# Performance work log

Hardware: AMD Instinct MI355X
Metric: run time of the kernel (lower is better)

## Reference

```python
import jax, jax.numpy as jnp
import numpy as np

VOCAB, EMB, HID, LAYERS, SEQ, BATCH = 10000, 1024, 1024, 2, 64, 64


def setup_inputs() -> dict:
    key = jax.random.key(0)
    ks = jax.random.split(key, 12)
    b = 1.0 / np.sqrt(HID)
    u = lambda k, shape, bd: jax.random.uniform(k, shape, jnp.float32, -bd, bd)
    return {
        "inputs": jax.random.randint(ks[0], (SEQ, BATCH), 0, VOCAB),
        "hidden": jnp.zeros((LAYERS, BATCH, HID), jnp.float32),
        "emb": u(ks[1], (VOCAB, EMB), 0.1),
        "W0": u(ks[2], (EMB, 3 * HID), b),
        "U0": u(ks[3], (HID, 3 * HID), b),
        "bw0": u(ks[4], (3 * HID,), b),
        "bu0": u(ks[5], (3 * HID,), b),
        "W1": u(ks[6], (HID, 3 * HID), b),
        "U1": u(ks[7], (HID, 3 * HID), b),
        "bw1": u(ks[8], (3 * HID,), b),
        "bu1": u(ks[9], (3 * HID,), b),
        "fcW": u(ks[10], (VOCAB, HID), 0.1),
        "fcb": jnp.zeros((VOCAB,), jnp.float32),
    }


def gru_cell(x, h, W, U, bw, bu):
    gx = x @ W + bw            # [B, 3H]
    gh = h @ U + bu            # [B, 3H]
    i_r, i_z, i_n = jnp.split(gx, 3, axis=1)
    h_r, h_z, h_n = jnp.split(gh, 3, axis=1)
    r = jax.nn.sigmoid(i_r + h_r)
    z = jax.nn.sigmoid(i_z + h_z)
    h_tilde = jnp.tanh(i_n + r * h_n)
    return (1.0 - z) * h + z * h_tilde


def reference(inputs, hidden, emb, W0, U0, bw0, bu0, W1, U1, bw1, bu1, fcW, fcb):
    # dp_keep_prob = 1.0 -> dropout is identity (eval-mode reference)
    def step(hid, tok):
        x = emb[tok]                                   # [B, EMB]
        h0 = gru_cell(x, hid[0], W0, U0, bw0, bu0)     # [B, H]
        h1 = gru_cell(h0, hid[1], W1, U1, bw1, bu1)    # [B, H]
        y = h1 @ fcW.T + fcb                           # [B, V]
        return jnp.stack([h0, h1]), y

    hidden_f, logits = jax.lax.scan(step, hidden, inputs)
    return logits, hidden_f
```

## Files before the change

kernel.cpp:

```cpp
#include <hip/hip_runtime.h>
#include <math.h>

#define SEQL 64
#define BATCHN 64
#define HID 1024
#define EMBD 1024
#define VOCAB 10000
#define G3 3072
#define NPAD 10240
#define AROWS 4096
#define HSLOT 65536

typedef float f4v __attribute__((ext_vector_type(4)));
typedef unsigned short us4 __attribute__((ext_vector_type(4)));
typedef unsigned short us8 __attribute__((ext_vector_type(8)));
typedef __bf16 bf8v __attribute__((ext_vector_type(8)));

__device__ __forceinline__ unsigned short f2bf(float f) {
    unsigned u = __float_as_uint(f);
    u += 0x7fffu + ((u >> 16) & 1u);
    return (unsigned short)(u >> 16);
}
__device__ __forceinline__ float bf2f(unsigned short h) {
    return __uint_as_float(((unsigned)h) << 16);
}
__device__ __forceinline__ void split2(float f, unsigned short &hi, unsigned short &lo) {
    hi = f2bf(f);
    lo = f2bf(f - bf2f(hi));
}
__device__ __forceinline__ f4v mfma16(us8 a, us8 b, f4v c) {
    return __builtin_amdgcn_mfma_f32_16x16x32_bf16(
        __builtin_bit_cast(bf8v, a), __builtin_bit_cast(bf8v, b), c, 0, 0, 0);
}
__device__ __forceinline__ float sigmoidf_(float x) { return 1.f / (1.f + expf(-x)); }

__device__ __forceinline__ size_t htile_off(int b, int j) {
    return ((size_t)((((b >> 4) * 32 + (j >> 5)) * 64) + ((j >> 3) & 3) * 16 + (b & 15))) * 8 + (j & 7);
}

__global__ __launch_bounds__(256)
void tile_weights_kernel(const float* __restrict__ U0, const float* __restrict__ W1,
                         const float* __restrict__ U1, const float* __restrict__ W0,
                         unsigned short* __restrict__ hi, unsigned short* __restrict__ lo)
{
    __shared__ float tile[32][65];
    const int mat = blockIdx.z;
    const float* src = (mat == 0) ? U0 : (mat == 1) ? W1 : (mat == 2) ? U1 : W0;
    const int n0 = blockIdx.x * 64, k0 = blockIdx.y * 32;
    const int t = threadIdx.x, tx = t & 63, ty = t >> 6;
#pragma unroll
    for (int s = 0; s < 8; s++)
        tile[ty * 8 + s][tx] = src[(size_t)(k0 + ty * 8 + s) * G3 + n0 + tx];
    __syncthreads();
    const int c = t >> 6, lane = t & 63, fr = lane & 15, kg = lane >> 4;
    const int cc = (n0 >> 4) + c;
    const size_t off = (((size_t)(mat * 192 + cc) * 32 + (k0 >> 5)) * 64 + lane) * 8;
    us8 h8, l8;
#pragma unroll
    for (int e = 0; e < 8; e++) {
        unsigned short a, b;
        split2(tile[kg * 8 + e][c * 16 + fr], a, b);
        h8[e] = a; l8[e] = b;
    }
    *(us8*)(hi + off) = h8;
    *(us8*)(lo + off) = l8;
}

__global__ void fc_pad_split_kernel(const float* __restrict__ fcW,
                                    unsigned short* __restrict__ hi, unsigned short* __restrict__ lo,
                                    const float* __restrict__ fcb, float* __restrict__ fcb_pad)
{
    size_t g = (size_t)blockIdx.x * 256 + threadIdx.x;
    if (g < NPAD) fcb_pad[g] = (g < VOCAB) ? fcb[g] : 0.f;
    size_t i = g * 4;
    size_t row = i >> 10;
    f4v v = {0.f, 0.f, 0.f, 0.f};
    if (row < VOCAB) v = *(const f4v*)(fcW + i);
    us4 h, l;
#pragma unroll
    for (int j = 0; j < 4; j++) { unsigned short a, b; split2(v[j], a, b); h[j] = a; l[j] = b; }
    *(us4*)(hi + i) = h;
    *(us4*)(lo + i) = l;
}

__global__ void small_prep_kernel(const float* __restrict__ hidden,
                                  unsigned short* __restrict__ h0th, unsigned short* __restrict__ h0tl,
                                  unsigned short* __restrict__ h1th, unsigned short* __restrict__ h1tl)
{
    int idx = blockIdx.x * 256 + threadIdx.x;
    if (idx < BATCHN * HID) {
        int b = idx >> 10, j = idx & 1023;
        size_t o = htile_off(b, j);
        unsigned short a1, b1;
        split2(hidden[idx], a1, b1);                 h0th[o] = a1; h0tl[o] = b1;
        split2(hidden[BATCHN * HID + idx], a1, b1);  h1th[o] = a1; h1tl[o] = b1;
    }
}

__global__ __launch_bounds__(256)
void gx0_gemm_kernel(const int* __restrict__ tok, const float* __restrict__ emb,
                     const unsigned short* __restrict__ Wthi, const unsigned short* __restrict__ Wtlo,
                     float* __restrict__ C)
{
    __shared__ unsigned short Ah[128][40], Al[128][40];
    const int bswz = blockIdx.x;
    const int xcd = bswz & 7, s = bswz >> 3;
    const int col0 = (xcd + 8 * (s >> 5)) * 128;
    const int row0 = (s & 31) * 128;
    const int tid = threadIdx.x;
    const int lane = tid & 63, wave = tid >> 6;
    const int wm = wave >> 1, wn = wave & 1;
    const int srow = tid >> 1;
    const int shalf = (tid & 1) * 16;

    const float* asrc = emb + (size_t)tok[row0 + srow] * EMBD + shalf;
    const int fr = lane & 15, fk = (lane >> 4) * 8;
    const int cc0 = (col0 >> 4) + wn * 4;

    f4v a[4];
#pragma unroll
    for (int q = 0; q < 4; q++) a[q] = *(const f4v*)(asrc + q * 4);

    f4v acc[4][4] = {};
    for (int k0 = 0; k0 < EMBD; k0 += 32) {
        __syncthreads();
        us8 ahv[2], alv[2];
#pragma unroll
        for (int q = 0; q < 4; q++)
#pragma unroll
            for (int j = 0; j < 4; j++) {
                unsigned short h, l;
                split2(a[q][j], h, l);
                ahv[q >> 1][(q & 1) * 4 + j] = h;
                alv[q >> 1][(q & 1) * 4 + j] = l;
            }
        *(us8*)(&Ah[srow][shalf]) = ahv[0];     *(us8*)(&Ah[srow][shalf + 8]) = ahv[1];
        *(us8*)(&Al[srow][shalf]) = alv[0];     *(us8*)(&Al[srow][shalf + 8]) = alv[1];
        __syncthreads();
        if (k0 + 32 < EMBD) {
#pragma unroll
            for (int q = 0; q < 4; q++) a[q] = *(const f4v*)(asrc + k0 + 32 + q * 4);
        }
        const int ks = k0 >> 5;
        us8 bfh[4], bfl[4];
#pragma unroll
        for (int n = 0; n < 4; n++) {
            const size_t bo = (((size_t)(3 * 192 + cc0 + n) * 32 + ks) * 64 + lane) * 8;
            bfh[n] = *(const us8*)(Wthi + bo);
            bfl[n] = *(const us8*)(Wtlo + bo);
        }
        us8 afh[4], afl[4];
#pragma unroll
        for (int m = 0; m < 4; m++) {
            afh[m] = *(const us8*)(&Ah[wm * 64 + m * 16 + fr][fk]);
            afl[m] = *(const us8*)(&Al[wm * 64 + m * 16 + fr][fk]);
        }
#pragma unroll
        for (int n = 0; n < 4; n++)
#pragma unroll
            for (int m = 0; m < 4; m++) {
                acc[m][n] = mfma16(afh[m], bfh[n], acc[m][n]);
                acc[m][n] = mfma16(afh[m], bfl[n], acc[m][n]);
                acc[m][n] = mfma16(afl[m], bfh[n], acc[m][n]);
            }
    }
    const int fq = lane >> 4;
#pragma unroll
    for (int m = 0; m < 4; m++)
#pragma unroll
        for (int n = 0; n < 4; n++)
#pragma unroll
            for (int i = 0; i < 4; i++) {
                int r = row0 + wm * 64 + m * 16 + fq * 4 + i;
                int c = col0 + wn * 64 + n * 16 + fr;
                C[(size_t)r * G3 + c] = acc[m][n][i];
            }
}

__global__ __launch_bounds__(512)
void logits_gemm_kernel(const unsigned short* __restrict__ h1t_hi, const unsigned short* __restrict__ h1t_lo,
                        const unsigned short* __restrict__ Bhi, const unsigned short* __restrict__ Blo,
                        const float* __restrict__ bias, float* __restrict__ C)
{
    __shared__ unsigned short Bh[128][40], Bl[128][40];
    const int bswz = blockIdx.x;
    const int xcd = bswz & 7, s = bswz >> 3;
    const int rt = xcd + 8 * (s / 80);
    const int col0 = (s % 80) * 128;
    const int row0 = rt * 256;
    const int t0 = row0 >> 6;
    const int tid = threadIdx.x;
    const int lane = tid & 63, wave = tid >> 6;
    const int wm = wave >> 1, wn = wave & 1;
    const int srow = tid >> 2;
    const int skseg = (tid & 3) * 8;

    const unsigned short* bh_src = Bhi + (size_t)(col0 + srow) * HID + skseg;
    const unsigned short* bl_src = Blo + (size_t)(col0 + srow) * HID + skseg;

    f4v acc[4][4] = {};
    us8 bh2 = *(const us8*)(bh_src);
    us8 bl2 = *(const us8*)(bl_src);

    const int fr = lane & 15, fk = (lane >> 4) * 8;
    const size_t abase = (size_t)(t0 + wm) * HSLOT + (size_t)lane * 8;

    for (int k0 = 0; k0 < HID; k0 += 32) {
        __syncthreads();
        *(us8*)(&Bh[srow][skseg]) = bh2;
        *(us8*)(&Bl[srow][skseg]) = bl2;
        __syncthreads();
        if (k0 + 32 < HID) {
            bh2 = *(const us8*)(bh_src + k0 + 32);
            bl2 = *(const us8*)(bl_src + k0 + 32);
        }
        const int ks = k0 >> 5;
        us8 afh[4], afl[4];
#pragma unroll
        for (int m = 0; m < 4; m++) {
            const size_t ao = abase + (size_t)(m * 32 + ks) * 512;
            afh[m] = *(const us8*)(h1t_hi + ao);
            afl[m] = *(const us8*)(h1t_lo + ao);
        }
#pragma unroll
        for (int n = 0; n < 4; n++) {
            us8 bfh = *(const us8*)(&Bh[wn * 64 + n * 16 + fr][fk]);
            us8 bfl = *(const us8*)(&Bl[wn * 64 + n * 16 + fr][fk]);
#pragma unroll
            for (int m = 0; m < 4; m++) {
                acc[m][n] = mfma16(afh[m], bfh, acc[m][n]);
                acc[m][n] = mfma16(afh[m], bfl, acc[m][n]);
                acc[m][n] = mfma16(afl[m], bfh, acc[m][n]);
            }
        }
    }
    const int fq = lane >> 4;
#pragma unroll
    for (int m = 0; m < 4; m++)
#pragma unroll
        for (int n = 0; n < 4; n++)
#pragma unroll
            for (int i = 0; i < 4; i++) {
                int r = row0 + wm * 64 + m * 16 + fq * 4 + i;
                int c = col0 + wn * 64 + n * 16 + fr;
                float v = acc[m][n][i] + bias[c];
                if (c < VOCAB) C[(size_t)r * VOCAB + c] = v;
            }
}

template <int T0, int T1>
__global__ __launch_bounds__(256)
void step_gemm_kernel(const unsigned short* __restrict__ h0hi, const unsigned short* __restrict__ h0lo,
                      const unsigned short* __restrict__ h1hi, const unsigned short* __restrict__ h1lo,
                      const unsigned short* __restrict__ Wthi, const unsigned short* __restrict__ Wtlo,
                      float* __restrict__ P)
{
    const int tid = threadIdx.x, lane = tid & 63, wave = tid >> 6;
    const int jc = blockIdx.x >> 3, kh = blockIdx.x & 7;
    const int ks = kh * 4 + wave;
    const size_t abase = ((size_t)ks * 64 + lane) * 8;

    f4v acc[9][4] = {};
    us8 ah[4], al[4];

    if (T0 < 6) {
#pragma unroll
        for (int m = 0; m < 4; m++) {
            ah[m] = *(const us8*)(h0hi + abase + (size_t)m * 16384);
            al[m] = *(const us8*)(h0lo + abase + (size_t)m * 16384);
        }
#pragma unroll
        for (int t2 = T0; t2 < ((T1 < 6) ? T1 : 6); ++t2) {
            const int mat = t2 / 3, g = t2 % 3;
            const size_t base = (((size_t)(mat * 192 + g * 64 + jc) * 32 + ks) * 64 + lane) * 8;
            us8 bh = *(const us8*)(Wthi + base);
            us8 bl = *(const us8*)(Wtlo + base);
#pragma unroll
            for (int m = 0; m < 4; ++m) {
                acc[t2][m] = mfma16(ah[m], bh, acc[t2][m]);
                acc[t2][m] = mfma16(ah[m], bl, acc[t2][m]);
                acc[t2][m] = mfma16(al[m], bh, acc[t2][m]);
            }
        }
    }
    if (T1 > 6) {
#pragma unroll
        for (int m = 0; m < 4; m++) {
            ah[m] = *(const us8*)(h1hi + abase + (size_t)m * 16384);
            al[m] = *(const us8*)(h1lo + abase + (size_t)m * 16384);
        }
#pragma unroll
        for (int t2 = 6; t2 < T1; ++t2) {
            const int g = t2 % 3;
            const size_t base = (((size_t)(2 * 192 + g * 64 + jc) * 32 + ks) * 64 + lane) * 8;
            us8 bh = *(const us8*)(Wthi + base);
            us8 bl = *(const us8*)(Wtlo + base);
#pragma unroll
            for (int m = 0; m < 4; ++m) {
                acc[t2][m] = mfma16(ah[m], bh, acc[t2][m]);
                acc[t2][m] = mfma16(ah[m], bl, acc[t2][m]);
                acc[t2][m] = mfma16(al[m], bh, acc[t2][m]);
            }
        }
    }

    __shared__ f4v red[4][2][4][64];
    const int rrow = (lane >> 4) * 4, rcol = lane & 15;
#pragma unroll
    for (int c = 0; c < 5; ++c) {
        const int ta = 2 * c, tb = 2 * c + 1;
        if (tb >= T0 && ta < T1) {
#pragma unroll
            for (int u = 0; u < 2; ++u) {
                const int t2 = 2 * c + u;
                if (t2 >= T0 && t2 < T1) {
#pragma unroll
                    for (int m = 0; m < 4; ++m)
                        red[wave][u][m][lane] = acc[t2][m];
                }
            }
            __syncthreads();
#pragma unroll
            for (int s2 = 0; s2 < 2; ++s2) {
                const int combo = wave * 2 + s2;
                const int u = combo >> 2, m = combo & 3;
                const int t2 = 2 * c + u;
                if (t2 >= T0 && t2 < T1) {
                    f4v v = (red[0][u][m][lane] + red[1][u][m][lane])
                          + (red[2][u][m][lane] + red[3][u][m][lane]);
#pragma unroll
                    for (int i = 0; i < 4; ++i)
                        P[(((size_t)kh * 9 + t2) * 64 + (m * 16 + rrow + i)) * 1024 + jc * 16 + rcol]
                            = v[i];
                }
            }
            __syncthreads();
        }
    }
}

template <int T0, int T1>
__global__ __launch_bounds__(256)
void step_reduce_kernel(const float* __restrict__ P, const float* __restrict__ gx0next,
                        const float* __restrict__ bw0, const float* __restrict__ bu0,
                        const float* __restrict__ bw1, const float* __restrict__ bu1,
                        const unsigned short* __restrict__ h0hi, const unsigned short* __restrict__ h0lo,
                        const unsigned short* __restrict__ h1hi, const unsigned short* __restrict__ h1lo,
                        unsigned short* __restrict__ h0o_hi, unsigned short* __restrict__ h0o_lo,
                        unsigned short* __restrict__ h1o_hi, unsigned short* __restrict__ h1o_lo,
                        float* __restrict__ outF)
{
    const int idx = blockIdx.x * 256 + threadIdx.x;
    const int b = idx >> 10, j = idx & 1023;
    float G[9];
#pragma unroll
    for (int t2 = T0; t2 < T1; t2++) {
        const float* p = P + ((size_t)t2 * 64 + b) * 1024 + j;
        float s0 = 0.f, s1 = 0.f;
#pragma unroll
        for (int kh = 0; kh < 4; kh++) {
            s0 += p[(size_t)(kh * 9) * 64 * 1024];
            s1 += p[(size_t)((kh + 4) * 9) * 64 * 1024];
        }
        G[t2] = s0 + s1;
    }
    const size_t po = htile_off(b, j);
    if (T0 == 0) {
        float sr  = gx0next[(size_t)b * G3 + j]            + bw0[j]           + G[0] + bu0[j];
        float sz  = gx0next[(size_t)b * G3 + HID + j]      + bw0[HID + j]     + G[1] + bu0[HID + j];
        float gxn = gx0next[(size_t)b * G3 + 2 * HID + j]  + bw0[2 * HID + j];
        float ghn = G[2] + bu0[2 * HID + j];
        float r = sigmoidf_(sr);
        float z = sigmoidf_(sz);
        float ht = tanhf(gxn + r * ghn);
        float hp = bf2f(h0hi[po]) + bf2f(h0lo[po]);
        float hn = (1.f - z) * hp + z * ht;
        unsigned short hh, hl2; split2(hn, hh, hl2);
        h0o_hi[po] = hh; h0o_lo[po] = hl2;
    }
    if (T1 > 3) {
        float sr  = G[3] + bw1[j]           + G[6] + bu1[j];
        float sz  = G[4] + bw1[HID + j]     + G[7] + bu1[HID + j];
        float gxn = G[5] + bw1[2 * HID + j];
        float ghn = G[8] + bu1[2 * HID + j];
        float r = sigmoidf_(sr);
        float z = sigmoidf_(sz);
        float ht = tanhf(gxn + r * ghn);
        float hp = bf2f(h1hi[po]) + bf2f(h1lo[po]);
        float hn = (1.f - z) * hp + z * ht;
        unsigned short hh, hl2; split2(hn, hh, hl2);
        h1o_hi[po] = hh; h1o_lo[po] = hl2;
        if (T0 == 3) {
            outF[(size_t)b * HID + j] = bf2f(h0hi[po]) + bf2f(h0lo[po]);
            outF[(size_t)BATCHN * HID + b * HID + j] = hn;
        }
    }
}

extern "C" void kernel_launch(void* const* d_in, const int* in_sizes, int n_in,
                              void* d_out, int out_size, void* d_ws, size_t ws_size,
                              hipStream_t stream)
{
    (void)in_sizes; (void)n_in; (void)out_size;
    const int*   tok    = (const int*)  d_in[0];
    const float* hidden = (const float*)d_in[1];
    const float* emb    = (const float*)d_in[2];
    const float* W0     = (const float*)d_in[3];
    const float* U0     = (const float*)d_in[4];
    const float* bw0    = (const float*)d_in[5];
    const float* bu0    = (const float*)d_in[6];
    const float* W1     = (const float*)d_in[7];
    const float* U1     = (const float*)d_in[8];
    const float* bw1    = (const float*)d_in[9];
    const float* bu1    = (const float*)d_in[10];
    const float* fcW    = (const float*)d_in[11];
    const float* fcb    = (const float*)d_in[12];
    float* out = (float*)d_out;

    char* wsp = (char*)d_ws;
    size_t used = 0;
    auto alloc = [&](size_t bytes) -> char* {
        char* p = wsp + used;
        used += (bytes + 255) & ~(size_t)255;
        return p;
    };
    unsigned short* Wt_hi = (unsigned short*)alloc((size_t)4 * G3 * HID * 2);
    unsigned short* Wt_lo = (unsigned short*)alloc((size_t)4 * G3 * HID * 2);
    float*          GX0   = (float*)alloc((size_t)AROWS * G3 * 4);
    unsigned short* H0Thi = (unsigned short*)alloc((size_t)SEQL * HSLOT * 2);
    unsigned short* H0Tlo = (unsigned short*)alloc((size_t)SEQL * HSLOT * 2);
    unsigned short* H1Thi = (unsigned short*)alloc((size_t)SEQL * HSLOT * 2);
    unsigned short* H1Tlo = (unsigned short*)alloc((size_t)SEQL * HSLOT * 2);
    float*          P     = (float*)alloc((size_t)8 * 9 * BATCHN * HID * 4);
    unsigned short* h0ith = (unsigned short*)alloc((size_t)HSLOT * 2);
    unsigned short* h0itl = (unsigned short*)alloc((size_t)HSLOT * 2);
    unsigned short* h1ith = (unsigned short*)alloc((size_t)HSLOT * 2);
    unsigned short* h1itl = (unsigned short*)alloc((size_t)HSLOT * 2);
    if (used > ws_size) return;

    unsigned short* fcWhi = Wt_hi;
    unsigned short* fcWlo = Wt_lo;
    float*          fcbp  = (float*)((char*)Wt_hi + (size_t)NPAD * HID * 2);

    float* outHid = out + (size_t)AROWS * VOCAB;

    tile_weights_kernel<<<dim3(48, 32, 4), 256, 0, stream>>>(U0, W1, U1, W0, Wt_hi, Wt_lo);
    small_prep_kernel<<<256, 256, 0, stream>>>(hidden, h0ith, h0itl, h1ith, h1itl);
    gx0_gemm_kernel<<<768, 256, 0, stream>>>(tok, emb, Wt_hi, Wt_lo, GX0);

    step_gemm_kernel<0, 3><<<512, 256, 0, stream>>>(
        h0ith, h0itl, h1ith, h1itl, Wt_hi, Wt_lo, P);
    step_reduce_kernel<0, 3><<<256, 256, 0, stream>>>(
        P, GX0, bw0, bu0, bw1, bu1,
        h0ith, h0itl, h1ith, h1itl,
        H0Thi, H0Tlo,
        H1Thi + (size_t)63 * HSLOT, H1Tlo + (size_t)63 * HSLOT,
        outHid);

    for (int t = 0; t < 63; t++) {
        const unsigned short* h0h = H0Thi + (size_t)t * HSLOT;
        const unsigned short* h0l = H0Tlo + (size_t)t * HSLOT;
        const unsigned short* a1h = (t == 0) ? h1ith : H1Thi + (size_t)(t - 1) * HSLOT;
        const unsigned short* a1l = (t == 0) ? h1itl : H1Tlo + (size_t)(t - 1) * HSLOT;
        step_gemm_kernel<0, 9><<<512, 256, 0, stream>>>(
            h0h, h0l, a1h, a1l, Wt_hi, Wt_lo, P);
        step_reduce_kernel<0, 9><<<256, 256, 0, stream>>>(
            P, GX0 + (size_t)(t + 1) * BATCHN * G3, bw0, bu0, bw1, bu1,
            h0h, h0l, a1h, a1l,
            H0Thi + (size_t)(t + 1) * HSLOT, H0Tlo + (size_t)(t + 1) * HSLOT,
            H1Thi + (size_t)t * HSLOT, H1Tlo + (size_t)t * HSLOT,
            outHid);
    }
    step_gemm_kernel<3, 9><<<512, 256, 0, stream>>>(
        H0Thi + (size_t)63 * HSLOT, H0Tlo + (size_t)63 * HSLOT,
        H1Thi + (size_t)62 * HSLOT, H1Tlo + (size_t)62 * HSLOT,
        Wt_hi, Wt_lo, P);
    step_reduce_kernel<3, 9><<<256, 256, 0, stream>>>(
        P, GX0, bw0, bu0, bw1, bu1,
        H0Thi + (size_t)63 * HSLOT, H0Tlo + (size_t)63 * HSLOT,
        H1Thi + (size_t)62 * HSLOT, H1Tlo + (size_t)62 * HSLOT,
        h0ith, h0itl,
        H1Thi + (size_t)63 * HSLOT, H1Tlo + (size_t)63 * HSLOT,
        outHid);

    fc_pad_split_kernel<<<NPAD, 256, 0, stream>>>(fcW, fcWhi, fcWlo, fcb, fcbp);
    logits_gemm_kernel<<<1280, 512, 0, stream>>>(
        H1Thi, H1Tlo, fcWhi, fcWlo, fcbp, out);
}
```

Baseline: 1.604 ms.

## Retile logits GEMM to 128x128 blocks with fragment-ordered LDS layout

The logits GEMM now uses 256-thread blocks on 128x128 output tiles instead of 512-thread blocks on 256x128 tiles, doubling the grid and changing the XCD swizzle so blocks sharing a column tile of fcW land on the same XCD. The B tile in shared memory is stored in MFMA fragment order, so each lane reads one contiguous us8 with no padding and fewer bank conflicts. Each thread now stages two B rows per k-step. The trade-off is less A reuse per block, since each block covers half as many rows.

```diff
diff --git a/kernel.cpp b/kernel.cpp
--- a/kernel.cpp
+++ b/kernel.cpp
@@ -177,42 +177,45 @@
             }
 }
 
-__global__ __launch_bounds__(512)
+__global__ __launch_bounds__(256)
 void logits_gemm_kernel(const unsigned short* __restrict__ h1t_hi, const unsigned short* __restrict__ h1t_lo,
                         const unsigned short* __restrict__ Bhi, const unsigned short* __restrict__ Blo,
                         const float* __restrict__ bias, float* __restrict__ C)
 {
-    __shared__ unsigned short Bh[128][40], Bl[128][40];
+    __shared__ us8 Bfh[512], Bfl[512];
     const int bswz = blockIdx.x;
     const int xcd = bswz & 7, s = bswz >> 3;
-    const int rt = xcd + 8 * (s / 80);
-    const int col0 = (s % 80) * 128;
-    const int row0 = rt * 256;
+    const int col0 = (xcd + 8 * (s >> 5)) * 128;
+    const int row0 = (s & 31) * 128;
     const int t0 = row0 >> 6;
     const int tid = threadIdx.x;
     const int lane = tid & 63, wave = tid >> 6;
     const int wm = wave >> 1, wn = wave & 1;
-    const int srow = tid >> 2;
-    const int skseg = (tid & 3) * 8;
-
-    const unsigned short* bh_src = Bhi + (size_t)(col0 + srow) * HID + skseg;
-    const unsigned short* bl_src = Blo + (size_t)(col0 + srow) * HID + skseg;
+
+    const int sfr = tid & 15, skg = (tid >> 4) & 3, sn = tid >> 6;
+    const size_t srow0 = (size_t)(col0 + sn * 16 + sfr) * HID + skg * 8;
+    const size_t srow1 = srow0 + (size_t)64 * HID;
+
+    us8 bh2[2], bl2[2];
+    bh2[0] = *(const us8*)(Bhi + srow0);
+    bh2[1] = *(const us8*)(Bhi + srow1);
+    bl2[0] = *(const us8*)(Blo + srow0);
+    bl2[1] = *(const us8*)(Blo + srow1);
 
     f4v acc[4][4] = {};
-    us8 bh2 = *(const us8*)(bh_src);
-    us8 bl2 = *(const us8*)(bl_src);
-
-    const int fr = lane & 15, fk = (lane >> 4) * 8;
+    const int fr = lane & 15;
     const size_t abase = (size_t)(t0 + wm) * HSLOT + (size_t)lane * 8;
 
     for (int k0 = 0; k0 < HID; k0 += 32) {
         __syncthreads();
-        *(us8*)(&Bh[srow][skseg]) = bh2;
-        *(us8*)(&Bl[srow][skseg]) = bl2;
+        Bfh[tid] = bh2[0];  Bfh[tid + 256] = bh2[1];
+        Bfl[tid] = bl2[0];  Bfl[tid + 256] = bl2[1];
         __syncthreads();
         if (k0 + 32 < HID) {
-            bh2 = *(const us8*)(bh_src + k0 + 32);
-            bl2 = *(const us8*)(bl_src + k0 + 32);
+            bh2[0] = *(const us8*)(Bhi + srow0 + k0 + 32);
+            bh2[1] = *(const us8*)(Bhi + srow1 + k0 + 32);
+            bl2[0] = *(const us8*)(Blo + srow0 + k0 + 32);
+            bl2[1] = *(const us8*)(Blo + srow1 + k0 + 32);
         }
         const int ks = k0 >> 5;
         us8 afh[4], afl[4];
@@ -224,8 +227,8 @@
         }
 #pragma unroll
         for (int n = 0; n < 4; n++) {
-            us8 bfh = *(const us8*)(&Bh[wn * 64 + n * 16 + fr][fk]);
-            us8 bfl = *(const us8*)(&Bl[wn * 64 + n * 16 + fr][fk]);
+            us8 bfh = Bfh[(wn * 4 + n) * 64 + lane];
+            us8 bfl = Bfl[(wn * 4 + n) * 64 + lane];
 #pragma unroll
             for (int m = 0; m < 4; m++) {
                 acc[m][n] = mfma16(afh[m], bfh, acc[m][n]);
@@ -484,6 +487,6 @@
         outHid);
 
     fc_pad_split_kernel<<<NPAD, 256, 0, stream>>>(fcW, fcWhi, fcWlo, fcb, fcbp);
-    logits_gemm_kernel<<<1280, 512, 0, stream>>>(
+    logits_gemm_kernel<<<2560, 256, 0, stream>>>(
         H1Thi, H1Tlo, fcWhi, fcWlo, fcbp, out);
 }
```

After: 1.563 ms. 1.03x faster.
